# Optimization experiments

Measured on AMD Instinct MI355X. Metric: run time of the kernel, lower is better.

Reference implementation:

```python
import jax, jax.numpy as jnp
import numpy as np

B, S, D, E, H = 4, 2048, 1024, 8, 4096

def setup_inputs() -> dict:
    key = jax.random.key(0)
    ks = jax.random.split(key, 7)
    scale_d = 1.0 / np.sqrt(D)
    scale_h = 1.0 / np.sqrt(H)
    return {
        "x": jax.random.normal(ks[0], (B, S, D), dtype=jnp.float32),
        "Wr": jax.random.uniform(ks[1], (D, E), jnp.float32, -scale_d, scale_d),
        "br": jnp.zeros((E,), jnp.float32),
        "W1": jax.random.uniform(ks[2], (E, D, H), jnp.float32, -scale_d, scale_d),
        "b1": jax.random.uniform(ks[3], (E, H), jnp.float32, -scale_d, scale_d),
        "W2": jax.random.uniform(ks[4], (E, H, D), jnp.float32, -scale_h, scale_h),
        "b2": jax.random.uniform(ks[5], (E, D), jnp.float32, -scale_h, scale_h),
    }

def reference(x, Wr, br, W1, b1, W2, b2):
    # Router: softmax then argmax (top-1). Note: original does NOT scale
    # expert output by the routing weight and never applies capacity drop.
    route_logits = jnp.einsum("bsd,de->bse", x, Wr) + br
    routing_weights = jax.nn.softmax(route_logits, axis=-1)
    selected_expert = jnp.argmax(routing_weights, axis=-1)  # [B, S] int

    num_experts = W1.shape[0]
    out = jnp.zeros_like(x)
    # Fixed small loop over experts (structurally distinct weight slices);
    # select-by-mask keeps shapes static under jit.
    for e in range(num_experts):
        h = jax.nn.gelu(jnp.einsum("bsd,dh->bsh", x, W1[e]) + b1[e], approximate=False)
        y = jnp.einsum("bsh,hd->bsd", h, W2[e]) + b2[e]
        out = jnp.where((selected_expert == e)[..., None], y, out)
    return out
```

## Files before the change

### kernel.cpp

```cpp
#include <hip/hip_runtime.h>
#include <math.h>

#define TOK   8192
#define DD    1024
#define EE    8
#define HH    4096
#define MAXROWS 9216
#define MAXMT 72

typedef unsigned short u16;
typedef unsigned int   u32;
typedef __bf16 bf16x8 __attribute__((ext_vector_type(8)));
typedef float  f32x4  __attribute__((ext_vector_type(4)));

__device__ __forceinline__ u16 f2bf(float f) {
  union { float f; u32 u; } v; v.f = f;
  u32 r = v.u + 0x7fffu + ((v.u >> 16) & 1u);
  return (u16)(r >> 16);
}

__device__ __forceinline__ void gload16(const void* g, void* l) {
  __builtin_amdgcn_global_load_lds(
      (const __attribute__((address_space(1))) void*)g,
      (__attribute__((address_space(3))) void*)l, 16, 0, 0);
}

__global__ void k_init(int* rowmap, int* counts, int* fill) {
  int i = blockIdx.x * 256 + threadIdx.x;
  if (i < MAXROWS) rowmap[i] = -1;
  if (blockIdx.x == 0 && threadIdx.x < EE) { counts[threadIdx.x] = 0; fill[threadIdx.x] = 0; }
}

__global__ __launch_bounds__(256)
void k_route(const float* __restrict__ x, const float* __restrict__ Wr,
             const float* __restrict__ br, int* __restrict__ eid, int* __restrict__ counts) {
  int t = blockIdx.x;
  const float* xr = x + (size_t)t * DD;
  float acc[EE];
  #pragma unroll
  for (int e = 0; e < EE; ++e) acc[e] = 0.f;
  for (int d = threadIdx.x; d < DD; d += 256) {
    float xv = xr[d];
    const float4* wrow = (const float4*)(Wr + (size_t)d * EE);
    float4 a = wrow[0], b = wrow[1];
    acc[0] += xv * a.x; acc[1] += xv * a.y; acc[2] += xv * a.z; acc[3] += xv * a.w;
    acc[4] += xv * b.x; acc[5] += xv * b.y; acc[6] += xv * b.z; acc[7] += xv * b.w;
  }
  #pragma unroll
  for (int e = 0; e < EE; ++e)
    for (int off = 32; off > 0; off >>= 1) acc[e] += __shfl_down(acc[e], off);
  __shared__ float red[4][EE];
  int w = threadIdx.x >> 6, lt = threadIdx.x & 63;
  if (lt == 0) {
    #pragma unroll
    for (int e = 0; e < EE; ++e) red[w][e] = acc[e];
  }
  __syncthreads();
  if (threadIdx.x == 0) {
    float best = -1e30f; int be = 0;
    #pragma unroll
    for (int e = 0; e < EE; ++e) {
      float v = red[0][e] + red[1][e] + red[2][e] + red[3][e] + br[e];
      if (v > best) { best = v; be = e; }
    }
    eid[t] = be;
    atomicAdd(&counts[be], 1);
  }
}

__global__ void k_scan(const int* __restrict__ counts, int* __restrict__ poff) {
  if (threadIdx.x == 0) {
    int off = 0; poff[0] = 0;
    for (int e = 0; e < EE; ++e) { off += ((counts[e] + 127) >> 7) << 7; poff[e + 1] = off; }
  }
}

__global__ void k_fillmap(const int* __restrict__ eid, const int* __restrict__ poff,
                          int* __restrict__ fill, int* __restrict__ rowmap) {
  int t = blockIdx.x * 256 + threadIdx.x;
  if (t < TOK) {
    int e = eid[t];
    int pos = atomicAdd(&fill[e], 1);
    rowmap[poff[e] + pos] = t;
  }
}

__global__ void k_convx(const float* __restrict__ x, u16* __restrict__ xb) {
  int i = blockIdx.x * 256 + threadIdx.x;
  float4 v = ((const float4*)x)[i];
  u32 p0 = (u32)f2bf(v.x) | ((u32)f2bf(v.y) << 16);
  u32 p1 = (u32)f2bf(v.z) | ((u32)f2bf(v.w) << 16);
  ((uint2*)xb)[i] = make_uint2(p0, p1);
}

__global__ __launch_bounds__(256)
void k_transpose(const float* __restrict__ W, u16* __restrict__ WT, int K, int N) {
  __shared__ float tile[32][33];
  int e = blockIdx.z;
  int n0 = blockIdx.x * 32, k0 = blockIdx.y * 32;
  const float* We = W + (size_t)e * K * N;
  u16* WTe = WT + (size_t)e * K * N;
  int tx = threadIdx.x & 31, ty = threadIdx.x >> 5;
  #pragma unroll
  for (int i = 0; i < 4; ++i)
    tile[ty + 8 * i][tx] = We[(size_t)(k0 + ty + 8 * i) * N + n0 + tx];
  __syncthreads();
  #pragma unroll
  for (int i = 0; i < 4; ++i)
    WTe[(size_t)(n0 + ty + 8 * i) * K + k0 + tx] = f2bf(tile[tx][ty + 8 * i]);
}

template <int KDIM, int NDIM, bool G2>
__global__ __launch_bounds__(256)
void k_gemm(const u16* __restrict__ Abase, const u16* __restrict__ WT,
            const float* __restrict__ bias, const int* __restrict__ poff,
            const int* __restrict__ rowmap, u16* __restrict__ hout,
            float* __restrict__ yout) {
  const int mt = blockIdx.y;
  const int mlimit = poff[EE];
  const int mbase = mt * 128;
  if (mbase >= mlimit) return;
  int e = 0;
  #pragma unroll
  for (int q = 1; q < EE; ++q) e += (mbase >= poff[q]) ? 1 : 0;

  const int nbase = blockIdx.x * 128;
  const int tid = threadIdx.x;
  const int w = tid >> 6;
  const int lt = tid & 63;
  const int wr = w >> 1, wc = w & 1;

  __shared__ u16 lsA[128 * 64];
  __shared__ u16 lsB[128 * 64];

  const int lrow = lt >> 3, lcol = lt & 7;
  const int cwz = lcol ^ lrow;

  const u16* wte = WT + (size_t)e * NDIM * KDIM;
  const u16* gA[4]; const u16* gB[4];
  #pragma unroll
  for (int q = 0; q < 4; ++q) {
    int rq = w * 32 + q * 8 + lrow;
    int arow;
    if (G2) { arow = mbase + rq; }
    else { arow = rowmap[mbase + rq]; if (arow < 0) arow = 0; }
    gA[q] = Abase + (size_t)arow * KDIM + cwz * 8;
    gB[q] = wte + (size_t)(nbase + rq) * KDIM + cwz * 8;
  }

  f32x4 acc[4][4] = {};

  const int KT = KDIM / 64;
  for (int bk = 0; bk < KT; ++bk) {
    __syncthreads();
    #pragma unroll
    for (int q = 0; q < 4; ++q) {
      gload16(gA[q] + bk * 64, &lsA[(w * 32 + q * 8) * 64]);
      gload16(gB[q] + bk * 64, &lsB[(w * 32 + q * 8) * 64]);
    }
    __syncthreads();
    #pragma unroll
    for (int s = 0; s < 2; ++s) {
      const int quad = lt >> 4;
      const int cc = s * 4 + quad;
      bf16x8 af[4], bfv[4];
      #pragma unroll
      for (int i = 0; i < 4; ++i) {
        int row = wr * 64 + i * 16 + (lt & 15);
        int phys = row * 8 + (cc ^ (row & 7));
        af[i] = *(const bf16x8*)&lsA[phys * 8];
      }
      #pragma unroll
      for (int j = 0; j < 4; ++j) {
        int n = wc * 64 + j * 16 + (lt & 15);
        int phys = n * 8 + (cc ^ (n & 7));
        bfv[j] = *(const bf16x8*)&lsB[phys * 8];
      }
      #pragma unroll
      for (int i = 0; i < 4; ++i)
        #pragma unroll
        for (int j = 0; j < 4; ++j)
          acc[i][j] = __builtin_amdgcn_mfma_f32_16x16x32_bf16(af[i], bfv[j], acc[i][j], 0, 0, 0);
    }
  }

  float bv[4];
  #pragma unroll
  for (int j = 0; j < 4; ++j)
    bv[j] = bias[(size_t)e * NDIM + nbase + wc * 64 + j * 16 + (lt & 15)];

  #pragma unroll
  for (int i = 0; i < 4; ++i) {
    int rowb = mbase + wr * 64 + i * 16 + (lt >> 4) * 4;
    #pragma unroll
    for (int r = 0; r < 4; ++r) {
      int row = rowb + r;
      if (G2) {
        int tok = rowmap[row];
        if (tok >= 0) {
          float* yp = yout + (size_t)tok * NDIM + nbase + wc * 64 + (lt & 15);
          #pragma unroll
          for (int j = 0; j < 4; ++j) yp[j * 16] = acc[i][j][r] + bv[j];
        }
      } else {
        u16* hp = hout + (size_t)row * NDIM + nbase + wc * 64 + (lt & 15);
        #pragma unroll
        for (int j = 0; j < 4; ++j) {
          float v = acc[i][j][r] + bv[j];
          v = 0.5f * v * (1.0f + erff(v * 0.70710678118654752f));
          hp[j * 16] = f2bf(v);
        }
      }
    }
  }
}

extern "C" void kernel_launch(void* const* d_in, const int* in_sizes, int n_in,
                              void* d_out, int out_size, void* d_ws, size_t ws_size,
                              hipStream_t stream) {
  const float* x  = (const float*)d_in[0];
  const float* Wr = (const float*)d_in[1];
  const float* br = (const float*)d_in[2];
  const float* W1 = (const float*)d_in[3];
  const float* b1 = (const float*)d_in[4];
  const float* W2 = (const float*)d_in[5];
  const float* b2 = (const float*)d_in[6];
  float* out = (float*)d_out;

  char* ws = (char*)d_ws;
  int* eid    = (int*)(ws + 0);
  int* counts = (int*)(ws + 32768);
  int* fill   = (int*)(ws + 32768 + 64);
  int* poff   = (int*)(ws + 32768 + 128);
  int* rowmap = (int*)(ws + 33024);
  u16* xbf    = (u16*)(ws + 69888);
  u16* w1t    = (u16*)(ws + 16847104);
  u16* w2t    = (u16*)(ws + 83955968);
  u16* hbuf   = (u16*)(ws + 151064832);

  k_init<<<MAXROWS / 256, 256, 0, stream>>>(rowmap, counts, fill);
  k_route<<<TOK, 256, 0, stream>>>(x, Wr, br, eid, counts);
  k_scan<<<1, 64, 0, stream>>>(counts, poff);
  k_fillmap<<<TOK / 256, 256, 0, stream>>>(eid, poff, fill, rowmap);
  k_convx<<<(TOK * DD / 4) / 256, 256, 0, stream>>>(x, xbf);
  k_transpose<<<dim3(HH / 32, DD / 32, EE), 256, 0, stream>>>(W1, w1t, DD, HH);
  k_transpose<<<dim3(DD / 32, HH / 32, EE), 256, 0, stream>>>(W2, w2t, HH, DD);
  k_gemm<DD, HH, false><<<dim3(HH / 128, MAXMT), 256, 0, stream>>>(xbf, w1t, b1, poff, rowmap, hbuf, nullptr);
  k_gemm<HH, DD, true><<<dim3(DD / 128, MAXMT), 256, 0, stream>>>(hbuf, w2t, b2, poff, rowmap, nullptr, out);
}
```

Baseline: 786.1 us.

## Double-buffer GEMM LDS loads, switch to 32x32 MFMA, fuse bf16 convert into router

The grouped expert GEMMs now use two LDS buffers with a K step of 32. The next tile's global-to-LDS loads are issued before computing on the current one, which removes one barrier per iteration and overlaps load latency with MFMA work. The 16x16x32 MFMA tiling is replaced by 32x32x16 MFMA with 2x2 accumulators per wave, and launch bounds request 3 blocks per CU. The router now handles one token per wave and also writes the bf16 copy of x, which removes the separate conversion kernel and a second read of x. The risks are higher register pressure from the occupancy hint and the smaller K step per barrier.

Measured after the change: 723.5 us. 8.0% less time.

```diff
diff --git a/kernel.cpp b/kernel.cpp
--- a/kernel.cpp
+++ b/kernel.cpp
@@ -11,7 +11,7 @@
 typedef unsigned short u16;
 typedef unsigned int   u32;
 typedef __bf16 bf16x8 __attribute__((ext_vector_type(8)));
-typedef float  f32x4  __attribute__((ext_vector_type(4)));
+typedef float  f32x16 __attribute__((ext_vector_type(16)));
 
 __device__ __forceinline__ u16 f2bf(float f) {
   union { float f; u32 u; } v; v.f = f;
@@ -33,34 +33,42 @@
 
 __global__ __launch_bounds__(256)
 void k_route(const float* __restrict__ x, const float* __restrict__ Wr,
-             const float* __restrict__ br, int* __restrict__ eid, int* __restrict__ counts) {
-  int t = blockIdx.x;
-  const float* xr = x + (size_t)t * DD;
+             const float* __restrict__ br, int* __restrict__ eid,
+             int* __restrict__ counts, u16* __restrict__ xb) {
+  int t = blockIdx.x * 4 + (threadIdx.x >> 6);
+  int lt = threadIdx.x & 63;
+  const float4* xr = (const float4*)(x + (size_t)t * DD);
+  u16* xbr = xb + (size_t)t * DD;
+  const float4* wrp = (const float4*)Wr;
   float acc[EE];
   #pragma unroll
   for (int e = 0; e < EE; ++e) acc[e] = 0.f;
-  for (int d = threadIdx.x; d < DD; d += 256) {
-    float xv = xr[d];
-    const float4* wrow = (const float4*)(Wr + (size_t)d * EE);
-    float4 a = wrow[0], b = wrow[1];
-    acc[0] += xv * a.x; acc[1] += xv * a.y; acc[2] += xv * a.z; acc[3] += xv * a.w;
-    acc[4] += xv * b.x; acc[5] += xv * b.y; acc[6] += xv * b.z; acc[7] += xv * b.w;
+  #pragma unroll
+  for (int i = 0; i < 4; ++i) {
+    int d4 = lt + 64 * i;
+    float4 v = xr[d4];
+    u32 p0 = (u32)f2bf(v.x) | ((u32)f2bf(v.y) << 16);
+    u32 p1 = (u32)f2bf(v.z) | ((u32)f2bf(v.w) << 16);
+    ((uint2*)xbr)[d4] = make_uint2(p0, p1);
+    float vv[4] = { v.x, v.y, v.z, v.w };
+    #pragma unroll
+    for (int dd = 0; dd < 4; ++dd) {
+      float xv = vv[dd];
+      float4 a = wrp[(size_t)(d4 * 4 + dd) * 2];
+      float4 b = wrp[(size_t)(d4 * 4 + dd) * 2 + 1];
+      acc[0] += xv * a.x; acc[1] += xv * a.y; acc[2] += xv * a.z; acc[3] += xv * a.w;
+      acc[4] += xv * b.x; acc[5] += xv * b.y; acc[6] += xv * b.z; acc[7] += xv * b.w;
+    }
   }
   #pragma unroll
   for (int e = 0; e < EE; ++e)
+    #pragma unroll
     for (int off = 32; off > 0; off >>= 1) acc[e] += __shfl_down(acc[e], off);
-  __shared__ float red[4][EE];
-  int w = threadIdx.x >> 6, lt = threadIdx.x & 63;
   if (lt == 0) {
-    #pragma unroll
-    for (int e = 0; e < EE; ++e) red[w][e] = acc[e];
-  }
-  __syncthreads();
-  if (threadIdx.x == 0) {
     float best = -1e30f; int be = 0;
     #pragma unroll
     for (int e = 0; e < EE; ++e) {
-      float v = red[0][e] + red[1][e] + red[2][e] + red[3][e] + br[e];
+      float v = acc[e] + br[e];
       if (v > best) { best = v; be = e; }
     }
     eid[t] = be;
@@ -83,14 +91,6 @@
     int pos = atomicAdd(&fill[e], 1);
     rowmap[poff[e] + pos] = t;
   }
-}
-
-__global__ void k_convx(const float* __restrict__ x, u16* __restrict__ xb) {
-  int i = blockIdx.x * 256 + threadIdx.x;
-  float4 v = ((const float4*)x)[i];
-  u32 p0 = (u32)f2bf(v.x) | ((u32)f2bf(v.y) << 16);
-  u32 p1 = (u32)f2bf(v.z) | ((u32)f2bf(v.w) << 16);
-  ((uint2*)xb)[i] = make_uint2(p0, p1);
 }
 
 __global__ __launch_bounds__(256)
@@ -111,15 +111,14 @@
 }
 
 template <int KDIM, int NDIM, bool G2>
-__global__ __launch_bounds__(256)
+__global__ __launch_bounds__(256, 3)
 void k_gemm(const u16* __restrict__ Abase, const u16* __restrict__ WT,
             const float* __restrict__ bias, const int* __restrict__ poff,
             const int* __restrict__ rowmap, u16* __restrict__ hout,
             float* __restrict__ yout) {
   const int mt = blockIdx.y;
-  const int mlimit = poff[EE];
   const int mbase = mt * 128;
-  if (mbase >= mlimit) return;
+  if (mbase >= poff[EE]) return;
   int e = 0;
   #pragma unroll
   for (int q = 1; q < EE; ++q) e += (mbase >= poff[q]) ? 1 : 0;
@@ -130,85 +129,90 @@
   const int lt = tid & 63;
   const int wr = w >> 1, wc = w & 1;
 
-  __shared__ u16 lsA[128 * 64];
-  __shared__ u16 lsB[128 * 64];
-
-  const int lrow = lt >> 3, lcol = lt & 7;
-  const int cwz = lcol ^ lrow;
-
-  const u16* wte = WT + (size_t)e * NDIM * KDIM;
-  const u16* gA[4]; const u16* gB[4];
-  #pragma unroll
-  for (int q = 0; q < 4; ++q) {
-    int rq = w * 32 + q * 8 + lrow;
-    int arow;
-    if (G2) { arow = mbase + rq; }
-    else { arow = rowmap[mbase + rq]; if (arow < 0) arow = 0; }
-    gA[q] = Abase + (size_t)arow * KDIM + cwz * 8;
-    gB[q] = wte + (size_t)(nbase + rq) * KDIM + cwz * 8;
-  }
-
-  f32x4 acc[4][4] = {};
-
-  const int KT = KDIM / 64;
+  __shared__ u16 lsA[2][128 * 32];
+  __shared__ u16 lsB[2][128 * 32];
+
+  const int srow = lt >> 2;
+  const int clog = (lt & 3) ^ (srow & 3);
+  int ar0, ar1;
+  if (G2) { ar0 = mbase + w * 16 + srow; ar1 = ar0 + 64; }
+  else {
+    ar0 = rowmap[mbase + w * 16 + srow];      if (ar0 < 0) ar0 = 0;
+    ar1 = rowmap[mbase + 64 + w * 16 + srow]; if (ar1 < 0) ar1 = 0;
+  }
+  const u16* gA0 = Abase + (size_t)ar0 * KDIM + clog * 8;
+  const u16* gA1 = Abase + (size_t)ar1 * KDIM + clog * 8;
+  const u16* wte = WT + (size_t)e * NDIM * KDIM + (size_t)nbase * KDIM;
+  const u16* gB0 = wte + (size_t)(w * 16 + srow) * KDIM + clog * 8;
+  const u16* gB1 = wte + (size_t)(64 + w * 16 + srow) * KDIM + clog * 8;
+
+  f32x16 acc[2][2] = {};
+
+  #define STAGE(buf, koff)                                          \
+    do {                                                            \
+      gload16(gA0 + (koff), &lsA[buf][(w * 16) * 32]);              \
+      gload16(gA1 + (koff), &lsA[buf][(64 + w * 16) * 32]);         \
+      gload16(gB0 + (koff), &lsB[buf][(w * 16) * 32]);              \
+      gload16(gB1 + (koff), &lsB[buf][(64 + w * 16) * 32]);         \
+    } while (0)
+
+  STAGE(0, 0);
+  const int KT = KDIM / 32;
   for (int bk = 0; bk < KT; ++bk) {
     __syncthreads();
-    #pragma unroll
-    for (int q = 0; q < 4; ++q) {
-      gload16(gA[q] + bk * 64, &lsA[(w * 32 + q * 8) * 64]);
-      gload16(gB[q] + bk * 64, &lsB[(w * 32 + q * 8) * 64]);
-    }
-    __syncthreads();
+    if (bk + 1 < KT) STAGE((bk + 1) & 1, (bk + 1) * 32);
+    const u16* A = lsA[bk & 1];
+    const u16* B = lsB[bk & 1];
     #pragma unroll
     for (int s = 0; s < 2; ++s) {
-      const int quad = lt >> 4;
-      const int cc = s * 4 + quad;
-      bf16x8 af[4], bfv[4];
+      bf16x8 af[2], bg[2];
       #pragma unroll
-      for (int i = 0; i < 4; ++i) {
-        int row = wr * 64 + i * 16 + (lt & 15);
-        int phys = row * 8 + (cc ^ (row & 7));
-        af[i] = *(const bf16x8*)&lsA[phys * 8];
+      for (int i = 0; i < 2; ++i) {
+        int row = wr * 64 + i * 32 + (lt & 31);
+        int phys = (s * 2 + (lt >> 5)) ^ (row & 3);
+        af[i] = *(const bf16x8*)&A[row * 32 + phys * 8];
       }
       #pragma unroll
-      for (int j = 0; j < 4; ++j) {
-        int n = wc * 64 + j * 16 + (lt & 15);
-        int phys = n * 8 + (cc ^ (n & 7));
-        bfv[j] = *(const bf16x8*)&lsB[phys * 8];
+      for (int j = 0; j < 2; ++j) {
+        int nn = wc * 64 + j * 32 + (lt & 31);
+        int phys = (s * 2 + (lt >> 5)) ^ (nn & 3);
+        bg[j] = *(const bf16x8*)&B[nn * 32 + phys * 8];
       }
       #pragma unroll
-      for (int i = 0; i < 4; ++i)
+      for (int i = 0; i < 2; ++i)
         #pragma unroll
-        for (int j = 0; j < 4; ++j)
-          acc[i][j] = __builtin_amdgcn_mfma_f32_16x16x32_bf16(af[i], bfv[j], acc[i][j], 0, 0, 0);
-    }
-  }
-
-  float bv[4];
-  #pragma unroll
-  for (int j = 0; j < 4; ++j)
-    bv[j] = bias[(size_t)e * NDIM + nbase + wc * 64 + j * 16 + (lt & 15)];
-
-  #pragma unroll
-  for (int i = 0; i < 4; ++i) {
-    int rowb = mbase + wr * 64 + i * 16 + (lt >> 4) * 4;
-    #pragma unroll
-    for (int r = 0; r < 4; ++r) {
-      int row = rowb + r;
+        for (int j = 0; j < 2; ++j)
+          acc[i][j] = __builtin_amdgcn_mfma_f32_32x32x16_bf16(af[i], bg[j], acc[i][j], 0, 0, 0);
+    }
+  }
+  #undef STAGE
+
+  float bv[2];
+  #pragma unroll
+  for (int j = 0; j < 2; ++j)
+    bv[j] = bias[(size_t)e * NDIM + nbase + wc * 64 + j * 32 + (lt & 31)];
+
+  #pragma unroll
+  for (int i = 0; i < 2; ++i) {
+    const int rbase = wr * 64 + i * 32 + 4 * (lt >> 5);
+    #pragma unroll
+    for (int r = 0; r < 16; ++r) {
+      const int rl = rbase + (r & 3) + 8 * (r >> 2);
+      const int grow = mbase + rl;
       if (G2) {
-        int tok = rowmap[row];
+        int tok = rowmap[grow];
         if (tok >= 0) {
-          float* yp = yout + (size_t)tok * NDIM + nbase + wc * 64 + (lt & 15);
+          float* yp = yout + (size_t)tok * NDIM + nbase + wc * 64 + (lt & 31);
           #pragma unroll
-          for (int j = 0; j < 4; ++j) yp[j * 16] = acc[i][j][r] + bv[j];
+          for (int j = 0; j < 2; ++j) yp[j * 32] = acc[i][j][r] + bv[j];
         }
       } else {
-        u16* hp = hout + (size_t)row * NDIM + nbase + wc * 64 + (lt & 15);
+        u16* hp = hout + (size_t)grow * NDIM + nbase + wc * 64 + (lt & 31);
         #pragma unroll
-        for (int j = 0; j < 4; ++j) {
+        for (int j = 0; j < 2; ++j) {
           float v = acc[i][j][r] + bv[j];
           v = 0.5f * v * (1.0f + erff(v * 0.70710678118654752f));
-          hp[j * 16] = f2bf(v);
+          hp[j * 32] = f2bf(v);
         }
       }
     }
@@ -239,10 +243,9 @@
   u16* hbuf   = (u16*)(ws + 151064832);
 
   k_init<<<MAXROWS / 256, 256, 0, stream>>>(rowmap, counts, fill);
-  k_route<<<TOK, 256, 0, stream>>>(x, Wr, br, eid, counts);
+  k_route<<<TOK / 4, 256, 0, stream>>>(x, Wr, br, eid, counts, xbf);
   k_scan<<<1, 64, 0, stream>>>(counts, poff);
   k_fillmap<<<TOK / 256, 256, 0, stream>>>(eid, poff, fill, rowmap);
-  k_convx<<<(TOK * DD / 4) / 256, 256, 0, stream>>>(x, xbf);
   k_transpose<<<dim3(HH / 32, DD / 32, EE), 256, 0, stream>>>(W1, w1t, DD, HH);
   k_transpose<<<dim3(DD / 32, HH / 32, EE), 256, 0, stream>>>(W2, w2t, HH, DD);
   k_gemm<DD, HH, false><<<dim3(HH / 128, MAXMT), 256, 0, stream>>>(xbf, w1t, b1, poff, rowmap, hbuf, nullptr);
```
